# Performance work log

Hardware: AMD Instinct MI355X
Metric: run time of the kernel (lower is better)

## Reference

```python
import jax, jax.numpy as jnp
import numpy as np

N = 1_000_000      # occupied input voxels
NREF = 400_000     # occupied reference (target) voxels on the stride-2 grid
CIN = 32
COUT = 64
G = 256            # input spatial grid extent per axis
B = 4              # batch size (ME batch index in coords[:, 0])
PRIME = 2654435761 # odd -> bijective multiplier mod 2^26


def _decode_np(ids, g):
    z = ids % g; ids = ids // g
    y = ids % g; ids = ids // g
    x = ids % g; b = ids // g
    return np.stack([b, x, y, z], axis=1).astype(np.int32)


def setup_inputs() -> dict:
    key = jax.random.key(0)
    k1, k2, k3 = jax.random.split(key, 3)
    # unique input voxel coordinates on a B x G^3 grid (bijection mod 2^26)
    ids_in = (np.arange(N, dtype=np.int64) * PRIME) % (B * G ** 3)
    coords = _decode_np(ids_in, G)                      # [N,4] (b,x,y,z), unique
    # unique reference coordinates on the stride-2 output grid
    gh = G // 2
    ids_ref = (np.arange(NREF, dtype=np.int64) * PRIME) % (B * gh ** 3)
    ref = _decode_np(ids_ref, gh)
    ref[:, 1:] *= 2                                     # ME tensor-stride-2 coords
    feats = jax.random.normal(k1, (N, CIN), jnp.float32)
    W = jax.random.normal(k2, (8, CIN, COUT), jnp.float32) * (1.0 / np.sqrt(8 * CIN))
    b = jax.random.normal(k3, (COUT,), jnp.float32) * 0.01
    return {"feats": feats, "W": W, "b": b,
            "coords": jnp.asarray(coords), "ref_coords": jnp.asarray(ref)}


def _ravel(c, step):
    # faithful to get_target_by_sp_tensor: batch-major ravel of 4 columns
    return c[:, 3] + c[:, 2] * step + c[:, 1] * step * step + c[:, 0] * step * step * step


def reference(feats, W, b, coords, ref_coords):
    n = coords.shape[0]
    # --- hash table of input voxels (sorted keys + permuted features) ---
    in_key = ((coords[:, 0] * G + coords[:, 1]) * G + coords[:, 2]) * G + coords[:, 3]
    order = jnp.argsort(in_key)
    skeys = in_key[order]
    sfeats = feats[order]
    # --- output coordinates: stride-2 downsample (kernel=2, stride=2) ---
    p = coords.at[:, 1:].set((coords[:, 1:] // 2) * 2)
    pkey = ((p[:, 0] * G + p[:, 1]) * G + p[:, 2]) * G + p[:, 3]
    out_key = jnp.unique(pkey, size=n, fill_value=-1)   # sorted, padded with -1
    valid = out_key >= 0
    ok = jnp.where(valid, out_key, 0)
    oz = ok % G; r = ok // G
    oy = r % G; r = r // G
    ox = r % G; ob = r // G
    out_coords = jnp.where(valid[:, None], jnp.stack([ob, ox, oy, oz], axis=1), -1)
    # --- sparse conv: gather the 2x2x2 children of each output voxel ---
    acc = jnp.zeros((n, W.shape[2]), feats.dtype)
    offsets = [(dx, dy, dz) for dx in (0, 1) for dy in (0, 1) for dz in (0, 1)]
    for i, (dx, dy, dz) in enumerate(offsets):
        ckey = out_key + dx * G * G + dy * G + dz
        idx = jnp.clip(jnp.searchsorted(skeys, ckey), 0, n - 1)
        found = (skeys[idx] == ckey) & valid
        f = jnp.where(found[:, None], sfeats[idx], 0.0)
        acc = acc + f @ W[i]
    out_feats = jnp.where(valid[:, None], acc + b, 0.0)
    # --- pruning mask: ravel + isin, faithful to get_target_by_sp_tensor ---
    step = jnp.maximum(out_coords.max(), ref_coords.max()).astype(jnp.int32) + 1
    min_value = jnp.minimum(out_coords.min(), ref_coords.min())
    shift = jnp.where(min_value < 0, -min_value, 0)
    oc = out_coords.at[:, 1:].add(shift)
    rc = ref_coords.at[:, 1:].add(shift)
    out1d = _ravel(oc, step)
    ref1d = _ravel(rc, step)
    sref = jnp.sort(ref1d)
    j = jnp.clip(jnp.searchsorted(sref, out1d), 0, sref.shape[0] - 1)
    mask = (sref[j] == out1d) & valid
    out_feats = jnp.where(mask[:, None], out_feats, 0.0)
    return out_coords, out_feats, mask
```

## Files before the change

kernel.cpp:

```cpp
#include <hip/hip_runtime.h>

#define WORDS_P  (1u << 18)
#define NBLK2    1024

typedef float f4_native __attribute__((ext_vector_type(4)));

__device__ __forceinline__ unsigned k23_of(int b, int x, int y, int z) {
  return ((unsigned)b << 21) | ((unsigned)(x >> 1) << 14) |
         ((unsigned)(y >> 1) << 7) | (unsigned)(z >> 1);
}

__global__ __launch_bounds__(256) void fill_ws(f4_native* __restrict__ wsz, size_t n4) {
  size_t stride = (size_t)gridDim.x * 256u;
  f4_native z = {0.f, 0.f, 0.f, 0.f};
  for (size_t i = (size_t)blockIdx.x * 256u + threadIdx.x; i < n4; i += stride)
    wsz[i] = z;
}

__global__ __launch_bounds__(256) void build_bm(const int4* __restrict__ coords, int n,
                                                const int4* __restrict__ ref, int nref,
                                                unsigned* __restrict__ parbm,
                                                unsigned* __restrict__ refbm) {
  unsigned tid = blockIdx.x * 256u + threadIdx.x;
  unsigned nthr = gridDim.x * 256u;
  for (unsigned i = tid; i < (unsigned)(n + nref); i += nthr) {
    if (i < (unsigned)n) {
      int4 c = coords[i];
      unsigned k = k23_of(c.x, c.y, c.z, c.w);
      atomicOr(&parbm[k >> 5], 1u << (k & 31));
    } else {
      int4 c = ref[i - (unsigned)n];
      unsigned k = k23_of(c.x, c.y, c.z, c.w);
      atomicOr(&refbm[k >> 5], 1u << (k & 31));
    }
  }
}

__global__ __launch_bounds__(256) void scan_emit(const unsigned* __restrict__ parbm,
                                                 unsigned* __restrict__ refbm,
                                                 unsigned long long* __restrict__ look,
                                                 unsigned* __restrict__ counter,
                                                 unsigned* __restrict__ maskpre,
                                                 unsigned* __restrict__ clist,
                                                 unsigned* __restrict__ mrow,
                                                 unsigned* __restrict__ rowinfo,
                                                 float4* __restrict__ out_coords,
                                                 float* __restrict__ out_mask) {
  __shared__ unsigned s[256];
  __shared__ unsigned aggP_s, aggM_s, basP_s, basM_s;
  unsigned t = threadIdx.x, blk = blockIdx.x;
  unsigned w = blk * 256u + t;
  unsigned pw = parbm[w];
  unsigned mw = pw & refbm[w];
  refbm[w] = mw;
  unsigned cp = __popc(pw), cm = __popc(mw);

  s[t] = cp; __syncthreads();
  for (int off = 128; off > 0; off >>= 1) { if (t < (unsigned)off) s[t] += s[t + off]; __syncthreads(); }
  if (t == 0) aggP_s = s[0];
  __syncthreads();
  s[t] = cm; __syncthreads();
  for (int off = 128; off > 0; off >>= 1) { if (t < (unsigned)off) s[t] += s[t + off]; __syncthreads(); }
  if (t == 0) aggM_s = s[0];
  __syncthreads();

  if (t == 0) {
    unsigned aggP = aggP_s, aggM = aggM_s;
    unsigned long long va = (1ULL << 62) | ((unsigned long long)aggP << 25) |
                            (unsigned long long)aggM;
    atomicExch(&look[blk], va);
    unsigned basP = 0, basM = 0;
    int p = (int)blk - 1;
    while (p >= 0) {
      unsigned long long u;
      do { u = atomicAdd(&look[p], 0ULL); } while ((u >> 62) == 0ULL);
      basP += (unsigned)((u >> 25) & 0x1FFFFFFu);
      basM += (unsigned)(u & 0x1FFFFFFu);
      if ((u >> 62) == 2ULL) break;
      p--;
    }
    unsigned long long vi = (2ULL << 62) |
        ((unsigned long long)(basP + aggP) << 25) | (unsigned long long)(basM + aggM);
    atomicExch(&look[blk], vi);
    basP_s = basP; basM_s = basM;
    if (blk == NBLK2 - 1u) {
      counter[0] = basM + aggM;
      counter[1] = basP + aggP;
    }
  }
  __syncthreads();
  unsigned basP = basP_s, basM = basM_s;

  s[t] = cp; __syncthreads();
  for (int off = 1; off < 256; off <<= 1) {
    unsigned v = (t >= (unsigned)off) ? s[t - off] : 0u;
    __syncthreads(); s[t] += v; __syncthreads();
  }
  unsigned ppre = basP + ((t == 0) ? 0u : s[t - 1]);
  __syncthreads();
  s[t] = cm; __syncthreads();
  for (int off = 1; off < 256; off <<= 1) {
    unsigned v = (t >= (unsigned)off) ? s[t - off] : 0u;
    __syncthreads(); s[t] += v; __syncthreads();
  }
  unsigned mpre = basM + ((t == 0) ? 0u : s[t - 1]);
  maskpre[w] = mpre;
  for (unsigned k = 0; k < cm * 8u; k++) clist[mpre * 8u + k] = 0u;

  unsigned r = ppre, j = mpre, bits = pw;
  while (bits) {
    unsigned b = (unsigned)__ffs((int)bits) - 1u;
    bits &= bits - 1u;
    unsigned k = (w << 5) | b;
    float bb = (float)(k >> 21);
    float x = (float)(((k >> 14) & 127u) << 1);
    float y = (float)(((k >> 7) & 127u) << 1);
    float z = (float)((k & 127u) << 1);
    out_coords[r] = make_float4(bb, x, y, z);
    bool masked = (mw >> b) & 1u;
    out_mask[r] = masked ? 1.0f : 0.0f;
    if (masked) { mrow[j] = r; rowinfo[r] = j + 1u; j++; }
    else rowinfo[r] = 0u;
    r++;
  }
}

__global__ __launch_bounds__(256) void scatter_tail(const int4* __restrict__ coords, int n,
                                                    const unsigned* __restrict__ maskbm,
                                                    const unsigned* __restrict__ maskpre,
                                                    const unsigned* __restrict__ counter,
                                                    unsigned* __restrict__ clist,
                                                    unsigned* __restrict__ rowinfo,
                                                    float4* __restrict__ out_coords,
                                                    float* __restrict__ out_mask,
                                                    int nbN) {
  if ((int)blockIdx.x < nbN) {
    int i = blockIdx.x * 256 + threadIdx.x;
    if (i >= n) return;
    int4 c = coords[i];
    unsigned k = k23_of(c.x, c.y, c.z, c.w);
    unsigned w = k >> 5, b = k & 31u;
    unsigned mw = maskbm[w];
    if ((mw >> b) & 1u) {
      unsigned j = maskpre[w] + __popc(mw & ((1u << b) - 1u));
      unsigned off = (((unsigned)c.y & 1u) << 2) | (((unsigned)c.z & 1u) << 1) |
                     ((unsigned)c.w & 1u);
      clist[j * 8u + off] = (unsigned)i + 1u;
    }
    return;
  }
  unsigned P = counter[1];
  unsigned idx = (blockIdx.x - nbN) * 256u + threadIdx.x;
  unsigned ntail = (unsigned)n - P;
  float4 m1 = make_float4(-1.f, -1.f, -1.f, -1.f);
  for (unsigned i = idx; i < ntail; i += 64u * 256u) {
    out_coords[P + i] = m1;
    out_mask[P + i] = 0.0f;
    rowinfo[P + i] = 0u;
  }
}

__global__ __launch_bounds__(1024, 8) void conv_fill(const float* __restrict__ feats,
                                                     const float* __restrict__ Wg,
                                                     const float* __restrict__ bias,
                                                     const unsigned* __restrict__ clist,
                                                     const unsigned* __restrict__ mrow,
                                                     const unsigned* __restrict__ rowinfo,
                                                     const unsigned* __restrict__ counter,
                                                     int n,
                                                     float* __restrict__ out_feats) {
  __shared__ float lw[16384];
  for (unsigned t = threadIdx.x; t < 4096u; t += 1024u)
    ((float4*)lw)[t] = ((const float4*)Wg)[t];
  __syncthreads();

  unsigned tid = blockIdx.x * 1024u + threadIdx.x;
  unsigned nthr = gridDim.x * 1024u;

  {
    f4_native z = {0.f, 0.f, 0.f, 0.f};
    size_t n4 = (size_t)n * 16u;
    f4_native* of = (f4_native*)out_feats;
    for (size_t i = tid; i < n4; i += nthr) {
      unsigned row = (unsigned)(i >> 4);
      if (rowinfo[row] == 0u) __builtin_nontemporal_store(z, &of[i]);
    }
  }

  unsigned lane = threadIdx.x & 63u;
  unsigned wave = blockIdx.x * 16u + (threadIdx.x >> 6);
  unsigned nwaves = gridDim.x * 16u;
  unsigned M = counter[0];
  float bv = bias[lane];
  for (unsigned j = wave; j < M; j += nwaves) {
    unsigned r = mrow[j];
    uint4 c0 = *(const uint4*)(clist + (size_t)j * 8u);
    uint4 c1 = *(const uint4*)(clist + (size_t)j * 8u + 4u);
    unsigned cs[8] = {c0.x, c0.y, c0.z, c0.w, c1.x, c1.y, c1.z, c1.w};
    float acc = bv;
#pragma unroll
    for (int i = 0; i < 8; i++) {
      unsigned v = (unsigned)__builtin_amdgcn_readfirstlane((int)cs[i]);
      if (v) {
        const float* f = feats + (size_t)(v - 1u) * 32u;
        const float* wl = lw + i * 2048 + lane;
#pragma unroll
        for (int k = 0; k < 32; k++) acc = fmaf(f[k], wl[k * 64], acc);
      }
    }
    out_feats[(size_t)r * 64u + lane] = acc;
  }
}

extern "C" void kernel_launch(void* const* d_in, const int* in_sizes, int n_in,
                              void* d_out, int out_size, void* d_ws, size_t ws_size,
                              hipStream_t stream) {
  const float* feats = (const float*)d_in[0];
  const float* W     = (const float*)d_in[1];
  const float* bias  = (const float*)d_in[2];
  const int4*  coords = (const int4*)d_in[3];
  const int4*  ref    = (const int4*)d_in[4];
  int N    = in_sizes[0] / 32;
  int NREF = in_sizes[4] / 4;

  float* out_coords = (float*)d_out;
  float* out_feats  = out_coords + (size_t)N * 4;
  float* out_mask   = out_feats + (size_t)N * 64;

  char* ws = (char*)d_ws;
  unsigned* parbm   = (unsigned*)(ws);
  unsigned* refbm   = (unsigned*)(ws + (1u << 20));
  unsigned long long* look = (unsigned long long*)(ws + (2u << 20));
  unsigned* counter = (unsigned*)(ws + (2u << 20) + 8192);
  unsigned* clist   = (unsigned*)(ws + (3u << 20));
  unsigned* maskpre = (unsigned*)(ws + (16u << 20));
  unsigned* mrow    = (unsigned*)(ws + (17u << 20));
  unsigned* rowinfo = (unsigned*)(ws + (19u << 20));

  int nbN = (N + 255) / 256;

  fill_ws<<<128, 256, 0, stream>>>((f4_native*)ws,
                                   ((size_t)(2u << 20) + 16384u) / 16u);
  build_bm<<<2048, 256, 0, stream>>>(coords, N, ref, NREF, parbm, refbm);
  scan_emit<<<NBLK2, 256, 0, stream>>>(parbm, refbm, look, counter, maskpre, clist,
                                       mrow, rowinfo, (float4*)out_coords, out_mask);
  scatter_tail<<<nbN + 64, 256, 0, stream>>>(coords, N, refbm, maskpre, counter,
                                             clist, rowinfo, (float4*)out_coords,
                                             out_mask, nbN);
  conv_fill<<<512, 1024, 0, stream>>>(feats, W, bias, clist, mrow, rowinfo, counter,
                                      N, out_feats);
}
```

Before: 161.8 us.

## Zero-fill output features and mask in build pass, drop rowinfo array

Moves the zeroing of out_feats and out_mask into the bitmap-build kernel as one unconditional nontemporal fill. This removes the per-row rowinfo array, its writes in scan_emit and scatter_tail, and the conditional zero pass in the conv kernel. The conv kernel now only writes masked rows. In exchange, every output row is written twice (zero, then result) and the fill runs after the atomic bitmap work in the same kernel.

Result: faster. 142.3 us (-12.0%).

```diff
diff --git a/kernel.cpp b/kernel.cpp
--- a/kernel.cpp
+++ b/kernel.cpp
@@ -17,10 +17,12 @@
     wsz[i] = z;
 }
 
-__global__ __launch_bounds__(256) void build_bm(const int4* __restrict__ coords, int n,
-                                                const int4* __restrict__ ref, int nref,
-                                                unsigned* __restrict__ parbm,
-                                                unsigned* __restrict__ refbm) {
+__global__ __launch_bounds__(256) void build_fill(const int4* __restrict__ coords, int n,
+                                                  const int4* __restrict__ ref, int nref,
+                                                  unsigned* __restrict__ parbm,
+                                                  unsigned* __restrict__ refbm,
+                                                  f4_native* __restrict__ ofm,
+                                                  size_t n4_ofm) {
   unsigned tid = blockIdx.x * 256u + threadIdx.x;
   unsigned nthr = gridDim.x * 256u;
   for (unsigned i = tid; i < (unsigned)(n + nref); i += nthr) {
@@ -34,6 +36,9 @@
       atomicOr(&refbm[k >> 5], 1u << (k & 31));
     }
   }
+  f4_native z = {0.f, 0.f, 0.f, 0.f};
+  for (size_t i = tid; i < n4_ofm; i += nthr)
+    __builtin_nontemporal_store(z, &ofm[i]);
 }
 
 __global__ __launch_bounds__(256) void scan_emit(const unsigned* __restrict__ parbm,
@@ -43,7 +48,6 @@
                                                  unsigned* __restrict__ maskpre,
                                                  unsigned* __restrict__ clist,
                                                  unsigned* __restrict__ mrow,
-                                                 unsigned* __restrict__ rowinfo,
                                                  float4* __restrict__ out_coords,
                                                  float* __restrict__ out_mask) {
   __shared__ unsigned s[256];
@@ -117,10 +121,10 @@
     float y = (float)(((k >> 7) & 127u) << 1);
     float z = (float)((k & 127u) << 1);
     out_coords[r] = make_float4(bb, x, y, z);
-    bool masked = (mw >> b) & 1u;
-    out_mask[r] = masked ? 1.0f : 0.0f;
-    if (masked) { mrow[j] = r; rowinfo[r] = j + 1u; j++; }
-    else rowinfo[r] = 0u;
+    if ((mw >> b) & 1u) {
+      out_mask[r] = 1.0f;
+      mrow[j++] = r;
+    }
     r++;
   }
 }
@@ -130,9 +134,7 @@
                                                     const unsigned* __restrict__ maskpre,
                                                     const unsigned* __restrict__ counter,
                                                     unsigned* __restrict__ clist,
-                                                    unsigned* __restrict__ rowinfo,
                                                     float4* __restrict__ out_coords,
-                                                    float* __restrict__ out_mask,
                                                     int nbN) {
   if ((int)blockIdx.x < nbN) {
     int i = blockIdx.x * 256 + threadIdx.x;
@@ -153,39 +155,20 @@
   unsigned idx = (blockIdx.x - nbN) * 256u + threadIdx.x;
   unsigned ntail = (unsigned)n - P;
   float4 m1 = make_float4(-1.f, -1.f, -1.f, -1.f);
-  for (unsigned i = idx; i < ntail; i += 64u * 256u) {
-    out_coords[P + i] = m1;
-    out_mask[P + i] = 0.0f;
-    rowinfo[P + i] = 0u;
-  }
-}
-
-__global__ __launch_bounds__(1024, 8) void conv_fill(const float* __restrict__ feats,
-                                                     const float* __restrict__ Wg,
-                                                     const float* __restrict__ bias,
-                                                     const unsigned* __restrict__ clist,
-                                                     const unsigned* __restrict__ mrow,
-                                                     const unsigned* __restrict__ rowinfo,
-                                                     const unsigned* __restrict__ counter,
-                                                     int n,
-                                                     float* __restrict__ out_feats) {
+  for (unsigned i = idx; i < ntail; i += 64u * 256u) out_coords[P + i] = m1;
+}
+
+__global__ __launch_bounds__(1024, 8) void conv_lds(const float* __restrict__ feats,
+                                                    const float* __restrict__ Wg,
+                                                    const float* __restrict__ bias,
+                                                    const unsigned* __restrict__ clist,
+                                                    const unsigned* __restrict__ mrow,
+                                                    const unsigned* __restrict__ counter,
+                                                    float* __restrict__ out_feats) {
   __shared__ float lw[16384];
   for (unsigned t = threadIdx.x; t < 4096u; t += 1024u)
     ((float4*)lw)[t] = ((const float4*)Wg)[t];
   __syncthreads();
-
-  unsigned tid = blockIdx.x * 1024u + threadIdx.x;
-  unsigned nthr = gridDim.x * 1024u;
-
-  {
-    f4_native z = {0.f, 0.f, 0.f, 0.f};
-    size_t n4 = (size_t)n * 16u;
-    f4_native* of = (f4_native*)out_feats;
-    for (size_t i = tid; i < n4; i += nthr) {
-      unsigned row = (unsigned)(i >> 4);
-      if (rowinfo[row] == 0u) __builtin_nontemporal_store(z, &of[i]);
-    }
-  }
 
   unsigned lane = threadIdx.x & 63u;
   unsigned wave = blockIdx.x * 16u + (threadIdx.x >> 6);
@@ -235,18 +218,17 @@
   unsigned* clist   = (unsigned*)(ws + (3u << 20));
   unsigned* maskpre = (unsigned*)(ws + (16u << 20));
   unsigned* mrow    = (unsigned*)(ws + (17u << 20));
-  unsigned* rowinfo = (unsigned*)(ws + (19u << 20));
 
   int nbN = (N + 255) / 256;
 
   fill_ws<<<128, 256, 0, stream>>>((f4_native*)ws,
                                    ((size_t)(2u << 20) + 16384u) / 16u);
-  build_bm<<<2048, 256, 0, stream>>>(coords, N, ref, NREF, parbm, refbm);
+  build_fill<<<2048, 256, 0, stream>>>(coords, N, ref, NREF, parbm, refbm,
+                                       (f4_native*)out_feats,
+                                       (size_t)N * 65u * 4u / 16u);
   scan_emit<<<NBLK2, 256, 0, stream>>>(parbm, refbm, look, counter, maskpre, clist,
-                                       mrow, rowinfo, (float4*)out_coords, out_mask);
+                                       mrow, (float4*)out_coords, out_mask);
   scatter_tail<<<nbN + 64, 256, 0, stream>>>(coords, N, refbm, maskpre, counter,
-                                             clist, rowinfo, (float4*)out_coords,
-                                             out_mask, nbN);
-  conv_fill<<<512, 1024, 0, stream>>>(feats, W, bias, clist, mrow, rowinfo, counter,
-                                      N, out_feats);
-}
+                                             clist, (float4*)out_coords, nbN);
+  conv_lds<<<512, 1024, 0, stream>>>(feats, W, bias, clist, mrow, counter, out_feats);
+}
```
